# Kernel tuning notes

Measured on AMD Instinct MI355X. Metric: run time of the kernel, lower is better.

## Reference

```python
import jax, jax.numpy as jnp
import numpy as np

N = 20000
E = 320000
H = 4
IN_DIM = 2000
# (in_dim, per-head out channels, concat) for each GATConv layer
LAYER_DIMS = [(2000, 128, True), (512, 64, True), (256, 32, True), (128, 64, False)]
NEG_SLOPE = 0.2  # PyG GATConv LeakyReLU slope


def setup_inputs() -> dict:
    key = jax.random.key(0)
    ks = jax.random.split(key, 2 + 4 * len(LAYER_DIMS))
    inp = {
        "x": jax.random.normal(ks[0], (N, IN_DIM), dtype=jnp.float32),
        "edge_index": jax.random.randint(ks[1], (2, E), 0, N, dtype=jnp.int64),
    }
    for i, (din, c, concat) in enumerate(LAYER_DIMS):
        k0, k1, k2, _ = jax.random.split(ks[2 + i], 4)
        inp[f"W{i}"] = (jax.random.normal(k0, (din, H * c), dtype=jnp.float32)
                         * (1.0 / np.sqrt(din)).astype(np.float32))
        inp[f"as{i}"] = jax.random.normal(k1, (H, c), dtype=jnp.float32) * 0.1
        inp[f"ad{i}"] = jax.random.normal(k2, (H, c), dtype=jnp.float32) * 0.1
        inp[f"b{i}"] = jnp.zeros((H * c if concat else c,), dtype=jnp.float32)
    return inp


def gat_conv(x, src, dst, W, att_src, att_dst, bias, concat):
    n, c = x.shape[0], W.shape[1] // H
    h = (x @ W).reshape(n, H, c)                      # (N,H,C) per-head features
    a_s = jnp.einsum("nhc,hc->nh", h, att_src)        # (N,H) source logits
    a_d = jnp.einsum("nhc,hc->nh", h, att_dst)        # (N,H) target logits
    e = a_s[src] + a_d[dst]                           # (E,H) per-edge logits
    e = jnp.where(e > 0, e, NEG_SLOPE * e)            # leaky_relu
    # segment softmax over edges sharing the same target node
    m = jax.ops.segment_max(e, dst, num_segments=n)   # (N,H)
    ex = jnp.exp(e - m[dst])
    denom = jax.ops.segment_sum(ex, dst, num_segments=n)
    alpha = ex / denom[dst]                           # (E,H)
    # weighted scatter-aggregate of source features
    out = jax.ops.segment_sum(alpha[:, :, None] * h[src], dst, num_segments=n)  # (N,H,C)
    out = out.reshape(n, H * c) if concat else out.mean(axis=1)
    return out + bias


def reference(x, edge_index, W0, as0, ad0, b0, W1, as1, ad1, b1,
              W2, as2, ad2, b2, W3, as3, ad3, b3):
    loops = jnp.arange(N, dtype=edge_index.dtype)
    src = jnp.concatenate([edge_index[0], loops])     # add self-loops (PyG default)
    dst = jnp.concatenate([edge_index[1], loops])
    params = [(W0, as0, ad0, b0), (W1, as1, ad1, b1), (W2, as2, ad2, b2), (W3, as3, ad3, b3)]
    h = x
    for i, (W, a_s, a_d, b) in enumerate(params):
        concat = LAYER_DIMS[i][2]
        h = gat_conv(h, src, dst, W, a_s, a_d, b, concat)
        if i < len(params) - 1:
            h = jax.nn.elu(h)  # dropout inactive in eval mode
    return h
```

## Files before the change

### kernel.cpp

```cpp
#include <hip/hip_runtime.h>
#include <hip/hip_bf16.h>

#define GN 20000
#define GE 320000
#define GETOT (GE + GN)
#define GH 4
#define NROW 20096

typedef __attribute__((ext_vector_type(8))) _Float16 f16x8;
typedef __attribute__((ext_vector_type(4))) float f32x4;

__global__ void detect_dtype_kernel(const void* __restrict__ ei, int* __restrict__ flag) {
    if (threadIdx.x == 0 && blockIdx.x == 0) {
        const long long* p = (const long long*)ei;
        int ok = 1;
        for (int i = 0; i < 16; ++i) {
            long long v = p[i];
            if (v < 0 || v >= GN) ok = 0;
        }
        *flag = ok;
    }
}

__device__ __forceinline__ int load_idx(const void* ei, int is64, long long pos) {
    if (is64) return (int)((const long long*)ei)[pos];
    return ((const int*)ei)[pos];
}

__global__ void hist_kernel(const void* __restrict__ ei, const int* __restrict__ flagp,
                            int* __restrict__ counts) {
    int e = blockIdx.x * blockDim.x + threadIdx.x;
    if (e >= GETOT) return;
    int d;
    if (e < GE) d = load_idx(ei, *flagp, (long long)GE + e);
    else        d = e - GE;
    atomicAdd(&counts[d], 1);
}

__global__ __launch_bounds__(1024) void scan_kernel(const int* __restrict__ counts,
                                                    int* __restrict__ offsets,
                                                    int* __restrict__ cursor) {
    __shared__ int sh[1024];
    const int tid = threadIdx.x;
    constexpr int CH = 20;
    const int base = tid * CH;
    int loc[CH];
    int sum = 0;
#pragma unroll
    for (int i = 0; i < CH; ++i) {
        int idx = base + i;
        int v = (idx < GN) ? counts[idx] : 0;
        loc[i] = sum;
        sum += v;
    }
    sh[tid] = sum;
    __syncthreads();
    for (int o = 1; o < 1024; o <<= 1) {
        int t = (tid >= o) ? sh[tid - o] : 0;
        __syncthreads();
        sh[tid] += t;
        __syncthreads();
    }
    const int excl = tid ? sh[tid - 1] : 0;
#pragma unroll
    for (int i = 0; i < CH; ++i) {
        int idx = base + i;
        if (idx < GN) {
            int o = excl + loc[i];
            offsets[idx] = o;
            cursor[idx]  = o;
        }
    }
    if (tid == 1023) offsets[GN] = sh[1023];
}

__global__ void scatter_kernel(const void* __restrict__ ei, const int* __restrict__ flagp,
                               int* __restrict__ cursor, int* __restrict__ csr_src) {
    int e = blockIdx.x * blockDim.x + threadIdx.x;
    if (e >= GETOT) return;
    int s, d;
    if (e < GE) {
        int is64 = *flagp;
        s = load_idx(ei, is64, e);
        d = load_idx(ei, is64, (long long)GE + e);
    } else {
        s = d = e - GE;
    }
    int pos = atomicAdd(&cursor[d], 1);
    csr_src[pos] = s;
}

__device__ __forceinline__ float h2f(unsigned u) {
    unsigned short us = (unsigned short)u;
    _Float16 h;
    __builtin_memcpy(&h, &us, 2);
    return (float)h;
}
__device__ __forceinline__ unsigned short f2h_bits(float v) {
    _Float16 h = (_Float16)v;
    unsigned short us;
    __builtin_memcpy(&us, &h, 2);
    return us;
}

__global__ void convert_wt(const float* __restrict__ W,
                           _Float16* __restrict__ thi,
                           int K, int N, int Kpad) {
    __shared__ float tile[32][33];
    int kb = blockIdx.x * 32, nb = blockIdx.y * 32;
    for (int i = threadIdx.y; i < 32; i += 8) {
        int k = kb + i, n = nb + threadIdx.x;
        tile[i][threadIdx.x] = (k < K) ? W[(size_t)k * N + n] : 0.f;
    }
    __syncthreads();
    for (int i = threadIdx.y; i < 32; i += 8) {
        int n = nb + i, k = kb + threadIdx.x;
        thi[(size_t)n * Kpad + k] = (_Float16)tile[threadIdx.x][i];
    }
}

__device__ __forceinline__ int swz(int a) { return a ^ (((a >> 6) & 7) << 4); }
__device__ __forceinline__ int invswz(int p) {
    int b8 = (p >> 8) & 1, b7 = (p >> 7) & 1;
    int a6 = ((p >> 6) & 1) ^ b8;
    int a5 = ((p >> 5) & 1) ^ b7;
    int a4 = ((p >> 4) & 1) ^ a6;
    return (p & ~0x70) | (a4 << 4) | (a5 << 5) | (a6 << 6);
}
__device__ __forceinline__ int swzA32(int a) { return a ^ (((a >> 7) & 7) << 4); }

#define GLDS16(gsrc, ldst) __builtin_amdgcn_global_load_lds( \
    (const __attribute__((address_space(1))) void*)(gsrc),   \
    (__attribute__((address_space(3))) void*)(ldst), 16, 0, 0)

template <int MODE, int CD>
__global__ __launch_bounds__(256, MODE == 1 ? 3 : 4) void gemm_f16(
        const void* __restrict__ Ap, int lda, int K,
        const _Float16* __restrict__ Whi,
        int Kpad, void* __restrict__ Cp, int M, int N, int NC,
        const float* __restrict__ att_s, const float* __restrict__ att_d,
        float* __restrict__ a_s, float* __restrict__ a_d) {
    constexpr int BUFB = (MODE == 1) ? 24576 : 16384;
    constexpr int WOFF = (MODE == 1) ? 16384 : 8192;
    __shared__ char lds[2 * BUFB];
    const int tid = threadIdx.x;

    const int nwg = gridDim.x;
    const int q = nwg >> 3, r = nwg & 7;
    const int xcd = blockIdx.x & 7, sub = blockIdx.x >> 3;
    const int orig = (xcd < r ? xcd * (q + 1) : r * (q + 1) + (xcd - r) * q) + sub;
    const int brow = (orig / NC) * 128;
    const int bcol = (orig % NC) * 128;

    const int lane = tid & 63, wid = tid >> 6;
    const int wr = wid >> 1, wc = wid & 1;
    const int l4 = lane & 15, kg = lane >> 4;

    int row8[2], ecol[2];
#pragma unroll
    for (int p = 0; p < 2; ++p) {
        int a = invswz(p * 4096 + tid * 16);
        row8[p] = a >> 6;
        ecol[p] = (a & 63) >> 1;
    }
    int rB[2];
#pragma unroll
    for (int p = 0; p < 2; ++p) rB[p] = bcol + row8[p];

    int rA2[2];
    int rA4[4], eA4[4];
    if constexpr (MODE == 1) {
#pragma unroll
        for (int p = 0; p < 4; ++p) {
            int a = swzA32(p * 4096 + tid * 16);
            int rr = brow + (a >> 7);
            rA4[p] = rr < M ? rr : M - 1;
            eA4[p] = (a & 127) >> 2;
        }
    } else {
#pragma unroll
        for (int p = 0; p < 2; ++p) rA2[p] = brow + row8[p];
    }
    const float*    A32 = (const float*)Ap;
    const _Float16* Af  = (const _Float16*)Ap;

    auto STAGE = [&](int buf, int k0) {
        char* bb = lds + buf * BUFB;
        if constexpr (MODE == 1) {
#pragma unroll
            for (int p = 0; p < 4; ++p) {
                int kk = k0 + eA4[p];
                if (kk >= K) kk = 0;
                GLDS16(A32 + (size_t)rA4[p] * lda + kk, bb + p * 4096 + tid * 16);
            }
        } else {
#pragma unroll
            for (int p = 0; p < 2; ++p)
                GLDS16(Af + (size_t)rA2[p] * lda + k0 + ecol[p], bb + p * 4096 + tid * 16);
        }
#pragma unroll
        for (int p = 0; p < 2; ++p)
            GLDS16(Whi + (size_t)rB[p] * Kpad + k0 + ecol[p], bb + WOFF + p * 4096 + tid * 16);
    };

    int aoff[4], boff[4];
#pragma unroll
    for (int m = 0; m < 4; ++m) {
        int row = wr * 64 + m * 16 + l4;
        aoff[m] = (MODE == 1) ? swzA32(row * 128 + kg * 32) : swz(row * 64 + kg * 16);
        boff[m] = swz((wc * 64 + m * 16 + l4) * 64 + kg * 16);
    }

    f32x4 acc[4][4];
#pragma unroll
    for (int m = 0; m < 4; ++m)
#pragma unroll
        for (int n = 0; n < 4; ++n) acc[m][n] = (f32x4)(0.f);

    const int nk = Kpad / 32;
    STAGE(0, 0);

    for (int t = 0; t < nk; ++t) {
        if (t + 1 < nk) {
            STAGE((t + 1) & 1, (t + 1) * 32);
            if constexpr (MODE == 1)
                asm volatile("s_waitcnt vmcnt(6)" ::: "memory");
            else
                asm volatile("s_waitcnt vmcnt(4)" ::: "memory");
        } else {
            asm volatile("s_waitcnt vmcnt(0)" ::: "memory");
        }
        __builtin_amdgcn_s_barrier();
        __builtin_amdgcn_sched_barrier(0);

        char* bb = lds + (t & 1) * BUFB;
        f16x8 av[4], wh[4];
        if constexpr (MODE == 1) {
            f32x4 u0[4], u1[4];
#pragma unroll
            for (int m = 0; m < 4; ++m) {
                u0[m] = *(const f32x4*)(bb + aoff[m]);
                u1[m] = *(const f32x4*)(bb + (aoff[m] ^ 16));
            }
            __builtin_amdgcn_sched_barrier(0);
#pragma unroll
            for (int n = 0; n < 4; ++n)
                wh[n] = *(const f16x8*)(bb + WOFF + boff[n]);
            __builtin_amdgcn_sched_barrier(0);
            asm volatile("s_waitcnt lgkmcnt(4)" ::: "memory");
            __builtin_amdgcn_sched_barrier(0);
#pragma unroll
            for (int m = 0; m < 4; ++m) {
                av[m][0] = (_Float16)u0[m].x; av[m][1] = (_Float16)u0[m].y;
                av[m][2] = (_Float16)u0[m].z; av[m][3] = (_Float16)u0[m].w;
                av[m][4] = (_Float16)u1[m].x; av[m][5] = (_Float16)u1[m].y;
                av[m][6] = (_Float16)u1[m].z; av[m][7] = (_Float16)u1[m].w;
            }
        } else {
#pragma unroll
            for (int m = 0; m < 4; ++m) av[m] = *(const f16x8*)(bb + aoff[m]);
#pragma unroll
            for (int n = 0; n < 4; ++n) wh[n] = *(const f16x8*)(bb + WOFF + boff[n]);
        }
        asm volatile("s_waitcnt lgkmcnt(0)" ::: "memory");
        __builtin_amdgcn_sched_barrier(0);

#pragma unroll
        for (int m = 0; m < 4; ++m)
#pragma unroll
            for (int n = 0; n < 4; ++n)
                acc[m][n] = __builtin_amdgcn_mfma_f32_16x16x32_f16(av[m], wh[n], acc[m][n], 0, 0, 0);
        __builtin_amdgcn_s_barrier();
    }

    float atS[4], atD[4];
    int   hn[4];
#pragma unroll
    for (int n = 0; n < 4; ++n) {
        int gc = bcol + wc * 64 + n * 16 + l4;
        int hd = gc / CD;
        hn[n]  = hd;
        atS[n] = att_s[hd * CD + (gc - hd * CD)];
        atD[n] = att_d[hd * CD + (gc - hd * CD)];
    }

#pragma unroll
    for (int m = 0; m < 4; ++m) {
        int gr0 = brow + wr * 64 + m * 16 + (lane >> 4) * 4;
#pragma unroll
        for (int rr2 = 0; rr2 < 4; ++rr2) {
            int gr = gr0 + rr2;
            float v0 = acc[m][0][rr2], v1 = acc[m][1][rr2];
            float v2 = acc[m][2][rr2], v3 = acc[m][3][rr2];
            if (gr < M) {
                size_t ob = (size_t)gr * N + bcol + wc * 64 + l4;
                _Float16* C16 = (_Float16*)Cp;
                C16[ob] = (_Float16)v0; C16[ob + 16] = (_Float16)v1;
                C16[ob + 32] = (_Float16)v2; C16[ob + 48] = (_Float16)v3;
            }
            float ps0 = v0 * atS[0] + v1 * atS[1];
            float ps1 = v2 * atS[2] + v3 * atS[3];
            float pd0 = v0 * atD[0] + v1 * atD[1];
            float pd1 = v2 * atD[2] + v3 * atD[3];
#pragma unroll
            for (int o2 = 1; o2 < 16; o2 <<= 1) {
                ps0 += __shfl_xor(ps0, o2);
                ps1 += __shfl_xor(ps1, o2);
                pd0 += __shfl_xor(pd0, o2);
                pd1 += __shfl_xor(pd1, o2);
            }
            if (l4 == 0 && gr < M) {
                if (hn[0] == hn[2]) {
                    atomicAdd(&a_s[gr * GH + hn[0]], ps0 + ps1);
                    atomicAdd(&a_d[gr * GH + hn[0]], pd0 + pd1);
                } else {
                    atomicAdd(&a_s[gr * GH + hn[0]], ps0);
                    atomicAdd(&a_s[gr * GH + hn[2]], ps1);
                    atomicAdd(&a_d[gr * GH + hn[0]], pd0);
                    atomicAdd(&a_d[gr * GH + hn[2]], pd1);
                }
            }
        }
    }
}

template <int C, int CPT, int BLOCK>
__global__ __launch_bounds__(BLOCK) void gat_aggregate_f16(
        const unsigned short* __restrict__ hfeat,
        const float* __restrict__ a_s,
        const float* __restrict__ a_d,
        const int* __restrict__ offsets,
        const int* __restrict__ csr_src,
        const float* __restrict__ bias,
        unsigned short* __restrict__ of16) {
    constexpr int HC = GH * C;
    static_assert(BLOCK * CPT == HC, "coverage");
    const int n     = blockIdx.x;
    const int tid   = threadIdx.x;
    const int start = offsets[n];
    const int end   = offsets[n + 1];

    __shared__ float s_m[GH];
    __shared__ float s_den[GH];
    __shared__ int   s_src[64];
    __shared__ float s_al[GH][68];

    const float4 ad4 = *(const float4*)(a_d + n * GH);
    const float adh[GH] = {ad4.x, ad4.y, ad4.z, ad4.w};

    if (tid < 64) {
        float lmax[GH], lsum[GH];
#pragma unroll
        for (int h = 0; h < GH; ++h) lmax[h] = -1e30f;
        for (int e = start + tid; e < end; e += 64) {
            int s = csr_src[e];
            float4 as4 = *(const float4*)(a_s + s * GH);
            float l[GH] = {as4.x + adh[0], as4.y + adh[1], as4.z + adh[2], as4.w + adh[3]};
#pragma unroll
            for (int h = 0; h < GH; ++h) {
                float ll = l[h] > 0.f ? l[h] : 0.2f * l[h];
                lmax[h] = fmaxf(lmax[h], ll);
            }
        }
#pragma unroll
        for (int h = 0; h < GH; ++h)
#pragma unroll
            for (int o = 32; o; o >>= 1) lmax[h] = fmaxf(lmax[h], __shfl_xor(lmax[h], o));
#pragma unroll
        for (int h = 0; h < GH; ++h) lsum[h] = 0.f;
        for (int e = start + tid; e < end; e += 64) {
            int s = csr_src[e];
            float4 as4 = *(const float4*)(a_s + s * GH);
            float l[GH] = {as4.x + adh[0], as4.y + adh[1], as4.z + adh[2], as4.w + adh[3]};
#pragma unroll
            for (int h = 0; h < GH; ++h) {
                float ll = l[h] > 0.f ? l[h] : 0.2f * l[h];
                lsum[h] += __expf(ll - lmax[h]);
            }
        }
#pragma unroll
        for (int h = 0; h < GH; ++h)
#pragma unroll
            for (int o = 32; o; o >>= 1) lsum[h] += __shfl_xor(lsum[h], o);
        if (tid == 0) {
#pragma unroll
            for (int h = 0; h < GH; ++h) { s_m[h] = lmax[h]; s_den[h] = lsum[h]; }
        }
    }
    __syncthreads();

    float mm[GH], inv[GH];
#pragma unroll
    for (int h = 0; h < GH; ++h) { mm[h] = s_m[h]; inv[h] = 1.0f / s_den[h]; }

    const int ch0 = tid * CPT;
    const int hd  = ch0 / C;
    float acc[CPT];
#pragma unroll
    for (int j = 0; j < CPT; ++j) acc[j] = 0.f;

    for (int e0 = start; e0 < end; e0 += 64) {
        __syncthreads();
        if (tid < 64) {
            bool vld = (e0 + tid) < end;
            int s = vld ? csr_src[e0 + tid] : n;
            s_src[tid] = s;
            float4 as4 = *(const float4*)(a_s + s * GH);
            float l[GH] = {as4.x + adh[0], as4.y + adh[1], as4.z + adh[2], as4.w + adh[3]};
#pragma unroll
            for (int h = 0; h < GH; ++h) {
                float ll = l[h] > 0.f ? l[h] : 0.2f * l[h];
                s_al[h][tid] = vld ? __expf(ll - mm[h]) * inv[h] : 0.f;
            }
        }
        __syncthreads();
        int cnt = end - e0; if (cnt > 64) cnt = 64;
        int cnt4 = (cnt + 3) & ~3;
        for (int i = 0; i < cnt4; i += 4) {
            int4   ss = *(const int4*)&s_src[i];
            float4 aa = *(const float4*)&s_al[hd][i];
            if constexpr (CPT == 4) {
                uint2 v0 = ((const uint2*)(hfeat + (size_t)ss.x * HC))[tid];
                uint2 v1 = ((const uint2*)(hfeat + (size_t)ss.y * HC))[tid];
                uint2 v2 = ((const uint2*)(hfeat + (size_t)ss.z * HC))[tid];
                uint2 v3 = ((const uint2*)(hfeat + (size_t)ss.w * HC))[tid];
                acc[0] = fmaf(aa.x, h2f(v0.x & 0xffff), acc[0]);
                acc[1] = fmaf(aa.x, h2f(v0.x >> 16),    acc[1]);
                acc[2] = fmaf(aa.x, h2f(v0.y & 0xffff), acc[2]);
                acc[3] = fmaf(aa.x, h2f(v0.y >> 16),    acc[3]);
                acc[0] = fmaf(aa.y, h2f(v1.x & 0xffff), acc[0]);
                acc[1] = fmaf(aa.y, h2f(v1.x >> 16),    acc[1]);
                acc[2] = fmaf(aa.y, h2f(v1.y & 0xffff), acc[2]);
                acc[3] = fmaf(aa.y, h2f(v1.y >> 16),    acc[3]);
                acc[0] = fmaf(aa.z, h2f(v2.x & 0xffff), acc[0]);
                acc[1] = fmaf(aa.z, h2f(v2.x >> 16),    acc[1]);
                acc[2] = fmaf(aa.z, h2f(v2.y & 0xffff), acc[2]);
                acc[3] = fmaf(aa.z, h2f(v2.y >> 16),    acc[3]);
                acc[0] = fmaf(aa.w, h2f(v3.x & 0xffff), acc[0]);
                acc[1] = fmaf(aa.w, h2f(v3.x >> 16),    acc[1]);
                acc[2] = fmaf(aa.w, h2f(v3.y & 0xffff), acc[2]);
                acc[3] = fmaf(aa.w, h2f(v3.y >> 16),    acc[3]);
            } else {
                unsigned v0 = ((const unsigned*)(hfeat + (size_t)ss.x * HC))[tid];
                unsigned v1 = ((const unsigned*)(hfeat + (size_t)ss.y * HC))[tid];
                unsigned v2 = ((const unsigned*)(hfeat + (size_t)ss.z * HC))[tid];
                unsigned v3 = ((const unsigned*)(hfeat + (size_t)ss.w * HC))[tid];
                acc[0] = fmaf(aa.x, h2f(v0 & 0xffff), acc[0]);
                acc[1] = fmaf(aa.x, h2f(v0 >> 16),    acc[1]);
                acc[0] = fmaf(aa.y, h2f(v1 & 0xffff), acc[0]);
                acc[1] = fmaf(aa.y, h2f(v1 >> 16),    acc[1]);
                acc[0] = fmaf(aa.z, h2f(v2 & 0xffff), acc[0]);
                acc[1] = fmaf(aa.z, h2f(v2 >> 16),    acc[1]);
                acc[0] = fmaf(aa.w, h2f(v3 & 0xffff), acc[0]);
                acc[1] = fmaf(aa.w, h2f(v3 >> 16),    acc[1]);
            }
        }
    }

    unsigned short hs[CPT];
#pragma unroll
    for (int j = 0; j < CPT; ++j) {
        float v = acc[j] + bias[ch0 + j];
        v = v > 0.f ? v : expm1f(v);
        hs[j] = f2h_bits(v);
    }
    unsigned short* op = of16 + (size_t)n * HC + ch0;
    if constexpr (CPT == 4) {
        uint2 hw = make_uint2((unsigned)hs[0] | ((unsigned)hs[1] << 16),
                              (unsigned)hs[2] | ((unsigned)hs[3] << 16));
        *(uint2*)op = hw;
    } else {
        *(unsigned*)op = (unsigned)hs[0] | ((unsigned)hs[1] << 16);
    }
}

__global__ __launch_bounds__(128) void gat_aggregate_final_f16(
        const unsigned short* __restrict__ hfeat,
        const float* __restrict__ a_s,
        const float* __restrict__ a_d,
        const int* __restrict__ offsets,
        const int* __restrict__ csr_src,
        const float* __restrict__ bias,
        float* __restrict__ outf) {
    constexpr int C = 64, HC = GH * C;
    const int n     = blockIdx.x;
    const int tid   = threadIdx.x;
    const int start = offsets[n];
    const int end   = offsets[n + 1];

    __shared__ float s_m[GH];
    __shared__ float s_den[GH];
    __shared__ int   s_src[64];
    __shared__ float s_al[GH][68];
    __shared__ float sacc[256];

    const float4 ad4 = *(const float4*)(a_d + n * GH);
    const float adh[GH] = {ad4.x, ad4.y, ad4.z, ad4.w};

    if (tid < 64) {
        float lmax[GH], lsum[GH];
#pragma unroll
        for (int h = 0; h < GH; ++h) lmax[h] = -1e30f;
        for (int e = start + tid; e < end; e += 64) {
            int s = csr_src[e];
            float4 as4 = *(const float4*)(a_s + s * GH);
            float l[GH] = {as4.x + adh[0], as4.y + adh[1], as4.z + adh[2], as4.w + adh[3]};
#pragma unroll
            for (int h = 0; h < GH; ++h) {
                float ll = l[h] > 0.f ? l[h] : 0.2f * l[h];
                lmax[h] = fmaxf(lmax[h], ll);
            }
        }
#pragma unroll
        for (int h = 0; h < GH; ++h)
#pragma unroll
            for (int o = 32; o; o >>= 1) lmax[h] = fmaxf(lmax[h], __shfl_xor(lmax[h], o));
#pragma unroll
        for (int h = 0; h < GH; ++h) lsum[h] = 0.f;
        for (int e = start + tid; e < end; e += 64) {
            int s = csr_src[e];
            float4 as4 = *(const float4*)(a_s + s * GH);
            float l[GH] = {as4.x + adh[0], as4.y + adh[1], as4.z + adh[2], as4.w + adh[3]};
#pragma unroll
            for (int h = 0; h < GH; ++h) {
                float ll = l[h] > 0.f ? l[h] : 0.2f * l[h];
                lsum[h] += __expf(ll - lmax[h]);
            }
        }
#pragma unroll
        for (int h = 0; h < GH; ++h)
#pragma unroll
            for (int o = 32; o; o >>= 1) lsum[h] += __shfl_xor(lsum[h], o);
        if (tid == 0) {
#pragma unroll
            for (int h = 0; h < GH; ++h) { s_m[h] = lmax[h]; s_den[h] = lsum[h]; }
        }
    }
    __syncthreads();

    float mm[GH], inv[GH];
#pragma unroll
    for (int h = 0; h < GH; ++h) { mm[h] = s_m[h]; inv[h] = 1.0f / s_den[h]; }

    const int hd = (2 * tid) / C;
    float acc0 = 0.f, acc1 = 0.f;

    for (int e0 = start; e0 < end; e0 += 64) {
        __syncthreads();
        if (tid < 64) {
            bool vld = (e0 + tid) < end;
            int s = vld ? csr_src[e0 + tid] : n;
            s_src[tid] = s;
            float4 as4 = *(const float4*)(a_s + s * GH);
            float l[GH] = {as4.x + adh[0], as4.y + adh[1], as4.z + adh[2], as4.w + adh[3]};
#pragma unroll
            for (int h = 0; h < GH; ++h) {
                float ll = l[h] > 0.f ? l[h] : 0.2f * l[h];
                s_al[h][tid] = vld ? __expf(ll - mm[h]) * inv[h] : 0.f;
            }
        }
        __syncthreads();
        int cnt = end - e0; if (cnt > 64) cnt = 64;
        int cnt4 = (cnt + 3) & ~3;
        for (int i = 0; i < cnt4; i += 4) {
            int4   ss = *(const int4*)&s_src[i];
            float4 aa = *(const float4*)&s_al[hd][i];
            unsigned v0 = ((const unsigned*)(hfeat + (size_t)ss.x * HC))[tid];
            unsigned v1 = ((const unsigned*)(hfeat + (size_t)ss.y * HC))[tid];
            unsigned v2 = ((const unsigned*)(hfeat + (size_t)ss.z * HC))[tid];
            unsigned v3 = ((const unsigned*)(hfeat + (size_t)ss.w * HC))[tid];
            acc0 = fmaf(aa.x, h2f(v0 & 0xffff), acc0);
            acc1 = fmaf(aa.x, h2f(v0 >> 16),    acc1);
            acc0 = fmaf(aa.y, h2f(v1 & 0xffff), acc0);
            acc1 = fmaf(aa.y, h2f(v1 >> 16),    acc1);
            acc0 = fmaf(aa.z, h2f(v2 & 0xffff), acc0);
            acc1 = fmaf(aa.z, h2f(v2 >> 16),    acc1);
            acc0 = fmaf(aa.w, h2f(v3 & 0xffff), acc0);
            acc1 = fmaf(aa.w, h2f(v3 >> 16),    acc1);
        }
    }

    sacc[2 * tid]     = acc0;
    sacc[2 * tid + 1] = acc1;
    __syncthreads();
    if (tid < C) {
        float v = 0.f;
#pragma unroll
        for (int h = 0; h < GH; ++h) v += sacc[h * C + tid];
        outf[(size_t)n * C + tid] = v * (1.0f / GH) + bias[tid];
    }
}

extern "C" void kernel_launch(void* const* d_in, const int* in_sizes, int n_in,
                              void* d_out, int out_size, void* d_ws, size_t ws_size,
                              hipStream_t stream) {
    const float* x  = (const float*)d_in[0];
    const void*  ei = d_in[1];
    const float* W[4]  = {(const float*)d_in[2],  (const float*)d_in[6],
                          (const float*)d_in[10], (const float*)d_in[14]};
    const float* AS[4] = {(const float*)d_in[3],  (const float*)d_in[7],
                          (const float*)d_in[11], (const float*)d_in[15]};
    const float* AD[4] = {(const float*)d_in[4],  (const float*)d_in[8],
                          (const float*)d_in[12], (const float*)d_in[16]};
    const float* BI[4] = {(const float*)d_in[5],  (const float*)d_in[9],
                          (const float*)d_in[13], (const float*)d_in[17]};

    char*  w   = (char*)d_ws;
    size_t off = 0;
    auto alloc = [&](size_t b) -> char* {
        char* p = w + off;
        off += (b + 255) & ~(size_t)255;
        return p;
    };
    int*   flag    = (int*)alloc(4);
    int*   counts  = (int*)alloc((GN + 1) * sizeof(int));
    int*   offsets = (int*)alloc((GN + 1) * sizeof(int));
    int*   cursor  = (int*)alloc(GN * sizeof(int));
    int*   csr_src = (int*)alloc((size_t)GETOT * sizeof(int));
    float* attb    = (float*)alloc((size_t)8 * GN * GH * sizeof(float));
    float* aS[4], *aD[4];
    for (int i = 0; i < 4; ++i) {
        aS[i] = attb + (size_t)(2 * i)     * GN * GH;
        aD[i] = attb + (size_t)(2 * i + 1) * GN * GH;
    }
    unsigned short* hA = (unsigned short*)alloc((size_t)NROW * 512 * 2);
    unsigned short* hB = (unsigned short*)alloc((size_t)NROW * 512 * 2);
    _Float16* wt   = (_Float16*)alloc((size_t)512 * 2016 * 2);
    (void)in_sizes; (void)n_in; (void)out_size; (void)ws_size;

    detect_dtype_kernel<<<1, 64, 0, stream>>>(ei, flag);
    hipMemsetAsync(counts, 0, (GN + 1) * sizeof(int), stream);
    hipMemsetAsync(attb, 0, (size_t)8 * GN * GH * sizeof(float), stream);
    int eblocks = (GETOT + 255) / 256;
    hist_kernel<<<eblocks, 256, 0, stream>>>(ei, flag, counts);
    scan_kernel<<<1, 1024, 0, stream>>>(counts, offsets, cursor);
    scatter_kernel<<<eblocks, 256, 0, stream>>>(ei, flag, cursor, csr_src);

    const dim3 tb(32, 8);
    const int NR = (GN + 127) / 128;

    convert_wt<<<dim3(2016 / 32, 512 / 32), tb, 0, stream>>>(W[0], wt, 2000, 512, 2016);
    gemm_f16<1, 128><<<NR * 4, 256, 0, stream>>>(x, 2000, 2000, wt, 2016, hA, GN, 512, 4,
                                                 AS[0], AD[0], aS[0], aD[0]);
    gat_aggregate_f16<128, 4, 128><<<GN, 128, 0, stream>>>(hA, aS[0], aD[0], offsets, csr_src,
                                                           BI[0], hB);
    convert_wt<<<dim3(512 / 32, 256 / 32), tb, 0, stream>>>(W[1], wt, 512, 256, 512);
    gemm_f16<0, 64><<<NR * 2, 256, 0, stream>>>(hB, 512, 512, wt, 512, hA, GN, 256, 2,
                                                AS[1], AD[1], aS[1], aD[1]);
    gat_aggregate_f16<64, 4, 64><<<GN, 64, 0, stream>>>(hA, aS[1], aD[1], offsets, csr_src,
                                                        BI[1], hB);
    convert_wt<<<dim3(256 / 32, 128 / 32), tb, 0, stream>>>(W[2], wt, 256, 128, 256);
    gemm_f16<0, 32><<<NR * 1, 256, 0, stream>>>(hB, 256, 256, wt, 256, hA, GN, 128, 1,
                                                AS[2], AD[2], aS[2], aD[2]);
    gat_aggregate_f16<32, 2, 64><<<GN, 64, 0, stream>>>(hA, aS[2], aD[2], offsets, csr_src,
                                                        BI[2], hB);
    convert_wt<<<dim3(128 / 32, 256 / 32), tb, 0, stream>>>(W[3], wt, 128, 256, 128);
    gemm_f16<0, 64><<<NR * 2, 256, 0, stream>>>(hB, 128, 128, wt, 128, hA, GN, 256, 2,
                                                AS[3], AD[3], aS[3], aD[3]);
    gat_aggregate_final_f16<<<GN, 128, 0, stream>>>(hA, aS[3], aD[3], offsets, csr_src,
                                                    BI[3], (float*)d_out);
}
```

Measured before the change: 386.4 us.

## Convert fp32 A to fp16 in registers before LDS store in first GEMM

```diff
diff --git a/kernel.cpp b/kernel.cpp
--- a/kernel.cpp
+++ b/kernel.cpp
@@ -127,21 +127,20 @@
     int a4 = ((p >> 4) & 1) ^ a6;
     return (p & ~0x70) | (a4 << 4) | (a5 << 5) | (a6 << 6);
 }
-__device__ __forceinline__ int swzA32(int a) { return a ^ (((a >> 7) & 7) << 4); }
 
 #define GLDS16(gsrc, ldst) __builtin_amdgcn_global_load_lds( \
     (const __attribute__((address_space(1))) void*)(gsrc),   \
     (__attribute__((address_space(3))) void*)(ldst), 16, 0, 0)
 
 template <int MODE, int CD>
-__global__ __launch_bounds__(256, MODE == 1 ? 3 : 4) void gemm_f16(
+__global__ __launch_bounds__(256, 4) void gemm_f16(
         const void* __restrict__ Ap, int lda, int K,
         const _Float16* __restrict__ Whi,
         int Kpad, void* __restrict__ Cp, int M, int N, int NC,
         const float* __restrict__ att_s, const float* __restrict__ att_d,
         float* __restrict__ a_s, float* __restrict__ a_d) {
-    constexpr int BUFB = (MODE == 1) ? 24576 : 16384;
-    constexpr int WOFF = (MODE == 1) ? 16384 : 8192;
+    constexpr int BUFB = 16384;
+    constexpr int WOFF = 8192;
     __shared__ char lds[2 * BUFB];
     const int tid = threadIdx.x;
 
@@ -163,51 +162,54 @@
         row8[p] = a >> 6;
         ecol[p] = (a & 63) >> 1;
     }
-    int rB[2];
-#pragma unroll
-    for (int p = 0; p < 2; ++p) rB[p] = bcol + row8[p];
-
-    int rA2[2];
-    int rA4[4], eA4[4];
-    if constexpr (MODE == 1) {
-#pragma unroll
-        for (int p = 0; p < 4; ++p) {
-            int a = swzA32(p * 4096 + tid * 16);
-            int rr = brow + (a >> 7);
-            rA4[p] = rr < M ? rr : M - 1;
-            eA4[p] = (a & 127) >> 2;
-        }
-    } else {
-#pragma unroll
-        for (int p = 0; p < 2; ++p) rA2[p] = brow + row8[p];
+    int rA[2], rB[2];
+#pragma unroll
+    for (int p = 0; p < 2; ++p) {
+        rA[p] = (MODE == 1) ? min(brow + row8[p], M - 1) : (brow + row8[p]);
+        rB[p] = bcol + row8[p];
     }
     const float*    A32 = (const float*)Ap;
     const _Float16* Af  = (const _Float16*)Ap;
 
-    auto STAGE = [&](int buf, int k0) {
+    auto STAGE_W = [&](int buf, int k0) {
         char* bb = lds + buf * BUFB;
-        if constexpr (MODE == 1) {
-#pragma unroll
-            for (int p = 0; p < 4; ++p) {
-                int kk = k0 + eA4[p];
-                if (kk >= K) kk = 0;
-                GLDS16(A32 + (size_t)rA4[p] * lda + kk, bb + p * 4096 + tid * 16);
-            }
-        } else {
-#pragma unroll
-            for (int p = 0; p < 2; ++p)
-                GLDS16(Af + (size_t)rA2[p] * lda + k0 + ecol[p], bb + p * 4096 + tid * 16);
-        }
 #pragma unroll
         for (int p = 0; p < 2; ++p)
             GLDS16(Whi + (size_t)rB[p] * Kpad + k0 + ecol[p], bb + WOFF + p * 4096 + tid * 16);
     };
+    auto STAGE_A16 = [&](int buf, int k0) {
+        char* bb = lds + buf * BUFB;
+#pragma unroll
+        for (int p = 0; p < 2; ++p)
+            GLDS16(Af + (size_t)rA[p] * lda + k0 + ecol[p], bb + p * 4096 + tid * 16);
+    };
+    auto LOADA32 = [&](float4 ar[2][2], int k0) {
+#pragma unroll
+        for (int p = 0; p < 2; ++p) {
+            int kk = k0 + ecol[p];
+            if (kk >= K) kk = 0;
+            const float* ap = A32 + (size_t)rA[p] * lda + kk;
+            ar[p][0] = *(const float4*)ap;
+            ar[p][1] = *(const float4*)(ap + 4);
+        }
+    };
+    auto WRITEA16 = [&](float4 ar[2][2], int buf) {
+        char* bb = lds + buf * BUFB;
+#pragma unroll
+        for (int p = 0; p < 2; ++p) {
+            f16x8 hv;
+            hv[0] = (_Float16)ar[p][0].x; hv[1] = (_Float16)ar[p][0].y;
+            hv[2] = (_Float16)ar[p][0].z; hv[3] = (_Float16)ar[p][0].w;
+            hv[4] = (_Float16)ar[p][1].x; hv[5] = (_Float16)ar[p][1].y;
+            hv[6] = (_Float16)ar[p][1].z; hv[7] = (_Float16)ar[p][1].w;
+            *(f16x8*)(bb + p * 4096 + tid * 16) = hv;
+        }
+    };
 
     int aoff[4], boff[4];
 #pragma unroll
     for (int m = 0; m < 4; ++m) {
-        int row = wr * 64 + m * 16 + l4;
-        aoff[m] = (MODE == 1) ? swzA32(row * 128 + kg * 32) : swz(row * 64 + kg * 16);
+        aoff[m] = swz((wr * 64 + m * 16 + l4) * 64 + kg * 16);
         boff[m] = swz((wc * 64 + m * 16 + l4) * 64 + kg * 16);
     }
 
@@ -218,59 +220,78 @@
         for (int n = 0; n < 4; ++n) acc[m][n] = (f32x4)(0.f);
 
     const int nk = Kpad / 32;
-    STAGE(0, 0);
-
-    for (int t = 0; t < nk; ++t) {
-        if (t + 1 < nk) {
-            STAGE((t + 1) & 1, (t + 1) * 32);
-            if constexpr (MODE == 1)
-                asm volatile("s_waitcnt vmcnt(6)" ::: "memory");
-            else
+
+    if constexpr (MODE == 1) {
+        float4 ar[2][2];
+        LOADA32(ar, 0);
+        STAGE_W(0, 0);
+        asm volatile("s_waitcnt vmcnt(2)" ::: "memory");
+        WRITEA16(ar, 0);
+
+        for (int t = 0; t < nk; ++t) {
+            float4 an[2][2];
+            if (t + 1 < nk) {
+                LOADA32(an, (t + 1) * 32);
                 asm volatile("s_waitcnt vmcnt(4)" ::: "memory");
-        } else {
-            asm volatile("s_waitcnt vmcnt(0)" ::: "memory");
-        }
-        __builtin_amdgcn_s_barrier();
-        __builtin_amdgcn_sched_barrier(0);
-
-        char* bb = lds + (t & 1) * BUFB;
-        f16x8 av[4], wh[4];
-        if constexpr (MODE == 1) {
-            f32x4 u0[4], u1[4];
-#pragma unroll
-            for (int m = 0; m < 4; ++m) {
-                u0[m] = *(const f32x4*)(bb + aoff[m]);
-                u1[m] = *(const f32x4*)(bb + (aoff[m] ^ 16));
-            }
+            } else {
+                asm volatile("s_waitcnt vmcnt(0)" ::: "memory");
+            }
+            asm volatile("s_waitcnt lgkmcnt(0)" ::: "memory");
+            __builtin_amdgcn_s_barrier();
             __builtin_amdgcn_sched_barrier(0);
-#pragma unroll
-            for (int n = 0; n < 4; ++n)
-                wh[n] = *(const f16x8*)(bb + WOFF + boff[n]);
+            if (t + 1 < nk) STAGE_W((t + 1) & 1, (t + 1) * 32);
+
+            char* bb = lds + (t & 1) * BUFB;
+            f16x8 av[4], wh[4];
+#pragma unroll
+            for (int m = 0; m < 4; ++m) av[m] = *(const f16x8*)(bb + aoff[m]);
+#pragma unroll
+            for (int n = 0; n < 4; ++n) wh[n] = *(const f16x8*)(bb + WOFF + boff[n]);
             __builtin_amdgcn_sched_barrier(0);
-            asm volatile("s_waitcnt lgkmcnt(4)" ::: "memory");
+            if (t + 1 < nk) {
+                asm volatile("s_waitcnt vmcnt(2)" ::: "memory");
+                __builtin_amdgcn_sched_barrier(0);
+                WRITEA16(an, (t + 1) & 1);
+                asm volatile("s_waitcnt lgkmcnt(2)" ::: "memory");
+            } else {
+                asm volatile("s_waitcnt lgkmcnt(0)" ::: "memory");
+            }
             __builtin_amdgcn_sched_barrier(0);
 #pragma unroll
-            for (int m = 0; m < 4; ++m) {
-                av[m][0] = (_Float16)u0[m].x; av[m][1] = (_Float16)u0[m].y;
-                av[m][2] = (_Float16)u0[m].z; av[m][3] = (_Float16)u0[m].w;
-                av[m][4] = (_Float16)u1[m].x; av[m][5] = (_Float16)u1[m].y;
-                av[m][6] = (_Float16)u1[m].z; av[m][7] = (_Float16)u1[m].w;
-            }
-        } else {
+            for (int m = 0; m < 4; ++m)
+#pragma unroll
+                for (int n = 0; n < 4; ++n)
+                    acc[m][n] = __builtin_amdgcn_mfma_f32_16x16x32_f16(av[m], wh[n], acc[m][n], 0, 0, 0);
+        }
+    } else {
+        STAGE_A16(0, 0);
+        STAGE_W(0, 0);
+        for (int t = 0; t < nk; ++t) {
+            if (t + 1 < nk) {
+                STAGE_A16((t + 1) & 1, (t + 1) * 32);
+                STAGE_W((t + 1) & 1, (t + 1) * 32);
+                asm volatile("s_waitcnt vmcnt(4)" ::: "memory");
+            } else {
+                asm volatile("s_waitcnt vmcnt(0)" ::: "memory");
+            }
+            __builtin_amdgcn_s_barrier();
+            __builtin_amdgcn_sched_barrier(0);
+
+            char* bb = lds + (t & 1) * BUFB;
+            f16x8 av[4], wh[4];
 #pragma unroll
             for (int m = 0; m < 4; ++m) av[m] = *(const f16x8*)(bb + aoff[m]);
 #pragma unroll
             for (int n = 0; n < 4; ++n) wh[n] = *(const f16x8*)(bb + WOFF + boff[n]);
-        }
-        asm volatile("s_waitcnt lgkmcnt(0)" ::: "memory");
-        __builtin_amdgcn_sched_barrier(0);
-
-#pragma unroll
-        for (int m = 0; m < 4; ++m)
-#pragma unroll
-            for (int n = 0; n < 4; ++n)
-                acc[m][n] = __builtin_amdgcn_mfma_f32_16x16x32_f16(av[m], wh[n], acc[m][n], 0, 0, 0);
-        __builtin_amdgcn_s_barrier();
+            asm volatile("s_waitcnt lgkmcnt(0)" ::: "memory");
+            __builtin_amdgcn_sched_barrier(0);
+#pragma unroll
+            for (int m = 0; m < 4; ++m)
+#pragma unroll
+                for (int n = 0; n < 4; ++n)
+                    acc[m][n] = __builtin_amdgcn_mfma_f32_16x16x32_f16(av[m], wh[n], acc[m][n], 0, 0, 0);
+            __builtin_amdgcn_s_barrier();
+        }
     }
 
     float atS[4], atD[4];
```

Result: slower. 471.2 us (+22.0%).
